# Optimization experiments

Measured on AMD Instinct MI355X. Metric: run time of the kernel, lower is better.

The kernel has to match this reference:

```python
import jax, jax.numpy as jnp
import numpy as np

N = 50000      # nodes
E = 800000     # edges (avg degree 16)
F_IN = 256
F_OUT = 256


def setup_inputs() -> dict:
    key = jax.random.key(0)
    ks = jax.random.split(key, 8)
    feature = jax.random.normal(ks[0], (N, F_IN), dtype=jnp.float32)
    e_w = jax.random.uniform(ks[1], (E, 1), dtype=jnp.float32)
    snorm_n = jnp.ones((N, 1), dtype=jnp.float32)
    snorm_e = jnp.ones((E, 1), dtype=jnp.float32)
    src = jax.random.randint(ks[2], (E,), 0, N, dtype=jnp.int32)
    dst = jax.random.randint(ks[3], (E,), 0, N, dtype=jnp.int32)
    scale = 1.0 / np.sqrt(F_IN)
    W_self = jax.random.normal(ks[4], (F_IN, F_OUT), dtype=jnp.float32) * scale
    W = jax.random.normal(ks[5], (F_IN, F_OUT), dtype=jnp.float32) * scale
    b = jax.random.normal(ks[6], (F_OUT,), dtype=jnp.float32) * scale
    return {"feature": feature, "e_w": e_w, "snorm_n": snorm_n,
            "snorm_e": snorm_e, "W_self": W_self, "W": W, "b": b,
            "src": src, "dst": dst}


def reference(feature, e_w, snorm_n, snorm_e, W_self, W, b, src, dst):
    n = feature.shape[0]
    ones_e = jnp.ones_like(src, dtype=feature.dtype)
    # self transform
    h_s = feature @ W_self                                   # [N, F_OUT]
    # source-side degree normalization: deg_out^{-1/2}
    out_deg = jnp.maximum(jax.ops.segment_sum(ones_e, src, num_segments=n), 1.0)
    feat = feature * (out_deg ** -0.5)[:, None]              # [N, F_IN]
    # message = h[src] * e_w, aggregated by sum into dst (u_mul_e + sum reduce)
    msgs = feat[src] * e_w                                   # [E, F_IN]
    agg = jax.ops.segment_sum(msgs, dst, num_segments=n)     # [N, F_IN]
    # neighbor transform + destination-side degree normalization
    h = agg @ W + b                                          # [N, F_OUT]
    in_deg = jnp.maximum(jax.ops.segment_sum(ones_e, dst, num_segments=n), 1.0)
    h = h * (in_deg ** -0.5)[:, None]
    return h_s + h, e_w
```

## Files before the change

kernel.cpp:

```cpp
#include <hip/hip_runtime.h>
#include <hip/hip_bf16.h>

#define N_NODES 50000
#define N_EDGES 800000

#define ROW_TILES    391
#define HIST_BLOCKS  782
#define GEMM_SPACE   1568
#define K1_BLOCKS    (HIST_BLOCKS + GEMM_SPACE)
#define WCONV_BLOCKS 512
#define SCAN_BLOCKS  196
#define EDGE_BLOCKS  782

typedef __bf16 bf16x8_t __attribute__((ext_vector_type(8)));
typedef float  f32x4_t  __attribute__((ext_vector_type(4)));
typedef unsigned short u16x8 __attribute__((ext_vector_type(8)));

__device__ __forceinline__ unsigned short f2bf(float x) {
  __hip_bfloat16 h = __float2bfloat16(x);
  return __builtin_bit_cast(unsigned short, h);
}
__device__ __forceinline__ float bf2f(unsigned short u) {
  unsigned int v = ((unsigned int)u) << 16;
  return __builtin_bit_cast(float, v);
}
__device__ __forceinline__ unsigned int pk2(float lo, float hi) {
  return ((unsigned int)f2bf(hi) << 16) | (unsigned int)f2bf(lo);
}

__global__ __launch_bounds__(256) void wconv_kernel(
    const float* __restrict__ Wself, const float* __restrict__ W,
    unsigned short* __restrict__ Bt)
{
  int idx = blockIdx.x * 256 + threadIdx.x;
  int n = idx >> 8, k = idx & 255;
  float v = (n < 256) ? Wself[k * 256 + n] : W[k * 256 + (n - 256)];
  Bt[idx] = f2bf(v);
}

__global__ __launch_bounds__(256, 4) void gemm_edge_kernel(
    const float* __restrict__ feature,
    const unsigned short* __restrict__ Bt,
    const float* __restrict__ e_w, const int* __restrict__ src, const int* __restrict__ dst,
    int* __restrict__ cnt_in, int* __restrict__ cnt_out,
    unsigned char* __restrict__ rank8, float* __restrict__ out1,
    unsigned short* __restrict__ hs16,
    unsigned char* __restrict__ y8)
{
  const int b   = blockIdx.x;
  const int tid = threadIdx.x;

  if (b < HIST_BLOCKS) {
    const int e0 = b * 1024 + tid;
#pragma unroll
    for (int k = 0; k < 4; ++k) {
      int e = e0 + k * 256;
      if (e < N_EDGES) {
        int s = src[e], d = dst[e];
        out1[e] = e_w[e];
        atomicAdd(&cnt_out[s], 1);
        rank8[e] = (unsigned char)atomicAdd(&cnt_in[d], 1);
      }
    }
    return;
  }

  const int u  = b - HIST_BLOCKS;
  const int q  = (u >> 3) & 3;
  const int t  = (u >> 5) * 8 + (((u & 7) + 6) & 7);
  if (t >= ROW_TILES) return;

  __shared__ __align__(16) unsigned short As[2][128 * 32];
  __shared__ __align__(16) unsigned short Bs[2][128 * 32];

  const int m0   = t * 128;
  const int bn0  = q * 128;
  const int lane = tid & 63;
  const int wave = tid >> 6;
  const int wm   = (wave & 1) * 64;
  const int wn   = (wave >> 1) * 64;
  const int fr   = lane & 15;
  const int fkc  = lane >> 4;

  const int ra = tid >> 1, ha = tid & 1;
  const int sA = (ra >> 1) & 3;
  const int arow = (m0 + ra < N_NODES) ? (m0 + ra) : 0;
  const float* aptr = feature + (size_t)arow * 256 + ha * 16;
  const int aw0 = ra * 32 + (((2 * ha) ^ sA) * 8);
  const int aw1 = ra * 32 + ((((2 * ha) | 1) ^ sA) * 8);

  f32x4_t acc[4][4] = {};

  {
#pragma unroll
    for (int i = 0; i < 2; ++i) {
      int r  = i * 64 + (tid >> 2);
      int cg = (tid & 3) ^ ((r >> 1) & 3);
      const unsigned short* gb = Bt + (size_t)(bn0 + r) * 256 + cg * 8;
      __builtin_amdgcn_global_load_lds((const __attribute__((address_space(1))) void*)gb,
                                       (__attribute__((address_space(3))) void*)&Bs[0][i * 2048 + wave * 512],
                                       16, 0, 0);
    }
    float4 a0 = *(const float4*)(aptr + 0);
    float4 a1 = *(const float4*)(aptr + 4);
    float4 a2 = *(const float4*)(aptr + 8);
    float4 a3 = *(const float4*)(aptr + 12);
    uint4 p0, p1;
    p0.x = pk2(a0.x, a0.y); p0.y = pk2(a0.z, a0.w);
    p0.z = pk2(a1.x, a1.y); p0.w = pk2(a1.z, a1.w);
    p1.x = pk2(a2.x, a2.y); p1.y = pk2(a2.z, a2.w);
    p1.z = pk2(a3.x, a3.y); p1.w = pk2(a3.z, a3.w);
    *(uint4*)&As[0][aw0] = p0;
    *(uint4*)&As[0][aw1] = p1;
  }
  __syncthreads();

#pragma unroll
  for (int s = 0; s < 8; ++s) {
    const int cb = s & 1, nb = cb ^ 1;
    float4 a0, a1, a2, a3;
    if (s < 7) {
      const int k0 = (s + 1) * 32;
#pragma unroll
      for (int i = 0; i < 2; ++i) {
        int r  = i * 64 + (tid >> 2);
        int cg = (tid & 3) ^ ((r >> 1) & 3);
        const unsigned short* gb = Bt + (size_t)(bn0 + r) * 256 + k0 + cg * 8;
        __builtin_amdgcn_global_load_lds((const __attribute__((address_space(1))) void*)gb,
                                         (__attribute__((address_space(3))) void*)&Bs[nb][i * 2048 + wave * 512],
                                         16, 0, 0);
      }
      a0 = *(const float4*)(aptr + k0 + 0);
      a1 = *(const float4*)(aptr + k0 + 4);
      a2 = *(const float4*)(aptr + k0 + 8);
      a3 = *(const float4*)(aptr + k0 + 12);
    }

    bf16x8_t af[4], bv[4];
#pragma unroll
    for (int i = 0; i < 4; ++i) {
      int R = wm + i * 16 + fr;
      af[i] = *(const bf16x8_t*)&As[cb][R * 32 + ((fkc ^ ((R >> 1) & 3)) * 8)];
    }
#pragma unroll
    for (int j = 0; j < 4; ++j) {
      int R = wn + j * 16 + fr;
      bv[j] = *(const bf16x8_t*)&Bs[cb][R * 32 + ((fkc ^ ((R >> 1) & 3)) * 8)];
    }
#pragma unroll
    for (int i = 0; i < 4; ++i)
#pragma unroll
      for (int j = 0; j < 4; ++j)
        acc[i][j] = __builtin_amdgcn_mfma_f32_16x16x32_bf16(af[i], bv[j], acc[i][j], 0, 0, 0);

    if (s < 7) {
      uint4 p0, p1;
      p0.x = pk2(a0.x, a0.y); p0.y = pk2(a0.z, a0.w);
      p0.z = pk2(a1.x, a1.y); p0.w = pk2(a1.z, a1.w);
      p1.x = pk2(a2.x, a2.y); p1.y = pk2(a2.z, a2.w);
      p1.z = pk2(a3.x, a3.y); p1.w = pk2(a3.z, a3.w);
      *(uint4*)&As[nb][aw0] = p0;
      *(uint4*)&As[nb][aw1] = p1;
      __syncthreads();
    }
  }

  if (q < 2) {
    const int cbase = q * 128 + wn + (lane & 15);
#pragma unroll
    for (int i = 0; i < 4; ++i) {
      int rowb = m0 + wm + i * 16 + (lane >> 4) * 4;
#pragma unroll
      for (int j = 0; j < 4; ++j) {
        int col = cbase + j * 16;
#pragma unroll
        for (int r = 0; r < 4; ++r) {
          int row = rowb + r;
          if (row < N_NODES)
            hs16[(size_t)row * 256 + col] = f2bf(acc[i][j][r]);
        }
      }
    }
  } else {
    const int cbase = (q - 2) * 128 + wn + (lane & 15);
#pragma unroll
    for (int i = 0; i < 4; ++i) {
      int rowb = m0 + wm + i * 16 + (lane >> 4) * 4;
#pragma unroll
      for (int j = 0; j < 4; ++j) {
        int col = cbase + j * 16;
#pragma unroll
        for (int r = 0; r < 4; ++r) {
          int row = rowb + r;
          if (row < N_NODES) {
            float ys = acc[i][j][r];
            unsigned int pk = (unsigned int)__builtin_amdgcn_cvt_pk_fp8_f32(ys, ys, 0, false);
            y8[(size_t)row * 256 + col] = (unsigned char)(pk & 0xffu);
          }
        }
      }
    }
  }
}

__global__ __launch_bounds__(256) void scan1_kernel(
    const int* __restrict__ cnt, int* __restrict__ sums)
{
  int idx = blockIdx.x * 256 + threadIdx.x;
  int v = (idx < N_NODES) ? cnt[idx] : 0;
#pragma unroll
  for (int d = 32; d; d >>= 1) v += __shfl_down(v, d);
  __shared__ int sm[4];
  if ((threadIdx.x & 63) == 0) sm[threadIdx.x >> 6] = v;
  __syncthreads();
  if (threadIdx.x == 0) sums[blockIdx.x] = sm[0] + sm[1] + sm[2] + sm[3];
}

__global__ __launch_bounds__(256) void scan2_kernel(int* __restrict__ sums)
{
  const int t = threadIdx.x;
  int v = (t < SCAN_BLOCKS) ? sums[t] : 0;
  __shared__ int sm[256];
  sm[t] = v;
  __syncthreads();
  for (int d = 1; d < 256; d <<= 1) {
    int u = (t >= d) ? sm[t - d] : 0;
    __syncthreads();
    sm[t] += u;
    __syncthreads();
  }
  if (t < SCAN_BLOCKS) sums[t] = sm[t] - v;
}

__global__ __launch_bounds__(256) void scan3_kernel(
    const int* __restrict__ cnt, const int* __restrict__ sums, int* __restrict__ off)
{
  const int t = threadIdx.x;
  int idx = blockIdx.x * 256 + t;
  int v = (idx < N_NODES) ? cnt[idx] : 0;
  __shared__ int sm[256];
  sm[t] = v;
  __syncthreads();
  for (int d = 1; d < 256; d <<= 1) {
    int u = (t >= d) ? sm[t - d] : 0;
    __syncthreads();
    sm[t] += u;
    __syncthreads();
  }
  if (idx <= N_NODES) off[idx] = sm[t] - v + sums[blockIdx.x];
}

__global__ __launch_bounds__(256) void scatter_kernel(
    const float* __restrict__ e_w, const int* __restrict__ src, const int* __restrict__ dst,
    const unsigned char* __restrict__ rank8, const int* __restrict__ off,
    unsigned int* __restrict__ csr)
{
  const int e0 = blockIdx.x * 1024 + threadIdx.x;
#pragma unroll
  for (int k = 0; k < 4; ++k) {
    int e = e0 + k * 256;
    if (e < N_EDGES) {
      int d = dst[e];
      int r = rank8[e];
      float w = e_w[e];
      int s = src[e];
      csr[off[d] + r] = ((unsigned int)f2bf(w) << 16) | (unsigned int)s;
    }
  }
}

__global__ __launch_bounds__(256) void agg_kernel(
    const unsigned char* __restrict__ y8, const unsigned int* __restrict__ csr,
    const int* __restrict__ off, const int* __restrict__ cnt_out,
    const unsigned short* __restrict__ hs16,
    const float* __restrict__ bias, float* __restrict__ out0)
{
  const int hw   = threadIdx.x >> 5;
  const int lane = threadIdx.x & 31;
  const int node = blockIdx.x * 8 + hw;
  if (node >= N_NODES) return;
  const int base = off[node];
  const int deg  = off[node + 1] - base;

  float a0 = 0.f, a1 = 0.f, a2 = 0.f, a3 = 0.f;
  float a4 = 0.f, a5 = 0.f, a6 = 0.f, a7 = 0.f;

  for (int bb = 0; bb < deg; bb += 32) {
    int idx = bb + lane;
    unsigned int ent = (idx < deg) ? csr[base + idx] : 0u;
    int   sl = (int)(ent & 0xffffu);
    float wl = bf2f((unsigned short)(ent >> 16));
    int co = cnt_out[sl]; if (co < 1) co = 1;
    wl *= rsqrtf((float)co);

#pragma unroll
    for (int t0 = 0; t0 < 32; t0 += 16) {
      if (bb + t0 >= deg) break;
#pragma unroll
      for (int t = 0; t < 16; ++t) {
        int eb = t0 + t;
        int   s = __shfl(sl, eb, 32);
        float w = __shfl(wl, eb, 32);
        uint2 u = *(const uint2*)(y8 + (size_t)s * 256 + lane * 8);
        a0 += w * __builtin_amdgcn_cvt_f32_fp8(u.x, 0);
        a1 += w * __builtin_amdgcn_cvt_f32_fp8(u.x, 1);
        a2 += w * __builtin_amdgcn_cvt_f32_fp8(u.x, 2);
        a3 += w * __builtin_amdgcn_cvt_f32_fp8(u.x, 3);
        a4 += w * __builtin_amdgcn_cvt_f32_fp8(u.y, 0);
        a5 += w * __builtin_amdgcn_cvt_f32_fp8(u.y, 1);
        a6 += w * __builtin_amdgcn_cvt_f32_fp8(u.y, 2);
        a7 += w * __builtin_amdgcn_cvt_f32_fp8(u.y, 3);
      }
    }
  }

  int dn = deg < 1 ? 1 : deg;
  float inv = rsqrtf((float)dn);
  size_t offo = (size_t)node * 256 + lane * 8;
  u16x8 hv = *(const u16x8*)(hs16 + offo);
  float4 b0 = *(const float4*)(bias + lane * 8);
  float4 b1 = *(const float4*)(bias + lane * 8 + 4);
  float4 o0, o1;
  o0.x = bf2f(hv[0]) + (a0 + b0.x) * inv;
  o0.y = bf2f(hv[1]) + (a1 + b0.y) * inv;
  o0.z = bf2f(hv[2]) + (a2 + b0.z) * inv;
  o0.w = bf2f(hv[3]) + (a3 + b0.w) * inv;
  o1.x = bf2f(hv[4]) + (a4 + b1.x) * inv;
  o1.y = bf2f(hv[5]) + (a5 + b1.y) * inv;
  o1.z = bf2f(hv[6]) + (a6 + b1.z) * inv;
  o1.w = bf2f(hv[7]) + (a7 + b1.w) * inv;
  *(float4*)(out0 + offo)     = o0;
  *(float4*)(out0 + offo + 4) = o1;
}

extern "C" void kernel_launch(void* const* d_in, const int* in_sizes, int n_in,
                              void* d_out, int out_size, void* d_ws, size_t ws_size,
                              hipStream_t stream) {
  const float* feature = (const float*)d_in[0];
  const float* e_w     = (const float*)d_in[1];
  const float* W_self  = (const float*)d_in[4];
  const float* W       = (const float*)d_in[5];
  const float* bias    = (const float*)d_in[6];
  const int*   src     = (const int*)d_in[7];
  const int*   dst     = (const int*)d_in[8];

  float* out0 = (float*)d_out;
  float* out1 = out0 + (size_t)N_NODES * 256;

  char* ws = (char*)d_ws;
  int*            cnt_in  = (int*)(ws + 0);
  int*            cnt_out = (int*)(ws + 262144);
  int*            off     = (int*)(ws + 524288);
  unsigned char*  rank8   = (unsigned char*)(ws + 786432);
  int*            sums    = (int*)(ws + 1638400);
  unsigned int*   csr     = (unsigned int*)(ws + 1835008);
  unsigned short* Bt      = (unsigned short*)(ws + 5242880);
  unsigned char*  y8      = (unsigned char*)(ws + 5767168);
  unsigned short* hs16    = (unsigned short*)(ws + 18567168);

  hipMemsetAsync(ws, 0, 524288, stream);

  wconv_kernel<<<WCONV_BLOCKS, 256, 0, stream>>>(W_self, W, Bt);
  gemm_edge_kernel<<<K1_BLOCKS, 256, 0, stream>>>(
      feature, Bt, e_w, src, dst, cnt_in, cnt_out, rank8, out1, hs16, y8);
  scan1_kernel<<<SCAN_BLOCKS, 256, 0, stream>>>(cnt_in, sums);
  scan2_kernel<<<1, 256, 0, stream>>>(sums);
  scan3_kernel<<<SCAN_BLOCKS, 256, 0, stream>>>(cnt_in, sums, off);
  scatter_kernel<<<EDGE_BLOCKS, 256, 0, stream>>>(e_w, src, dst, rank8, off, csr);
  agg_kernel<<<(N_NODES + 7) / 8, 256, 0, stream>>>(y8, csr, off, cnt_out, hs16, bias, out0);
}
```

Measured before the change: 283.5 us.

## Drop LDS staging in fused GEMM, load MFMA fragments directly from global

Removes the shared-memory double buffer and barriers from the GEMM part of the fused kernel. Each wave now loads its A (fp32, converted to bf16) and B fragments straight from global memory into registers. Histogram blocks are also interleaved with GEMM blocks in a 48-block pattern instead of all running first. This cuts LDS traffic and syncs and frees LDS for occupancy, at the cost of redundant global/L2 reads, since fragments are no longer shared across waves, and less latency hiding.

```diff
diff --git a/kernel.cpp b/kernel.cpp
--- a/kernel.cpp
+++ b/kernel.cpp
@@ -5,9 +5,7 @@
 #define N_EDGES 800000
 
 #define ROW_TILES    391
-#define HIST_BLOCKS  782
-#define GEMM_SPACE   1568
-#define K1_BLOCKS    (HIST_BLOCKS + GEMM_SPACE)
+#define K1_BLOCKS    2352
 #define WCONV_BLOCKS 512
 #define SCAN_BLOCKS  196
 #define EDGE_BLOCKS  782
@@ -15,6 +13,7 @@
 typedef __bf16 bf16x8_t __attribute__((ext_vector_type(8)));
 typedef float  f32x4_t  __attribute__((ext_vector_type(4)));
 typedef unsigned short u16x8 __attribute__((ext_vector_type(8)));
+typedef unsigned int   u32x4 __attribute__((ext_vector_type(4)));
 
 __device__ __forceinline__ unsigned short f2bf(float x) {
   __hip_bfloat16 h = __float2bfloat16(x);
@@ -26,6 +25,12 @@
 }
 __device__ __forceinline__ unsigned int pk2(float lo, float hi) {
   return ((unsigned int)f2bf(hi) << 16) | (unsigned int)f2bf(lo);
+}
+__device__ __forceinline__ bf16x8_t cvt8(float4 lo, float4 hi) {
+  u32x4 u;
+  u.x = pk2(lo.x, lo.y); u.y = pk2(lo.z, lo.w);
+  u.z = pk2(hi.x, hi.y); u.w = pk2(hi.z, hi.w);
+  return __builtin_bit_cast(bf16x8_t, u);
 }
 
 __global__ __launch_bounds__(256) void wconv_kernel(
@@ -49,9 +54,14 @@
 {
   const int b   = blockIdx.x;
   const int tid = threadIdx.x;
-
-  if (b < HIST_BLOCKS) {
-    const int e0 = b * 1024 + tid;
+  const int w   = b / 48;
+  const int o   = (b % 48) >> 3;
+  const int r   = b & 7;
+
+  if (o == 2 || o == 5) {
+    const int h = w * 16 + r + ((o == 5) ? 8 : 0);
+    if (h >= EDGE_BLOCKS) return;
+    const int e0 = h * 1024 + tid;
 #pragma unroll
     for (int k = 0; k < 4; ++k) {
       int e = e0 + k * 256;
@@ -65,13 +75,9 @@
     return;
   }
 
-  const int u  = b - HIST_BLOCKS;
-  const int q  = (u >> 3) & 3;
-  const int t  = (u >> 5) * 8 + (((u & 7) + 6) & 7);
+  const int q = o - (o > 2 ? 1 : 0);
+  const int t = w * 8 + r;
   if (t >= ROW_TILES) return;
-
-  __shared__ __align__(16) unsigned short As[2][128 * 32];
-  __shared__ __align__(16) unsigned short Bs[2][128 * 32];
 
   const int m0   = t * 128;
   const int bn0  = q * 128;
@@ -82,87 +88,37 @@
   const int fr   = lane & 15;
   const int fkc  = lane >> 4;
 
-  const int ra = tid >> 1, ha = tid & 1;
-  const int sA = (ra >> 1) & 3;
-  const int arow = (m0 + ra < N_NODES) ? (m0 + ra) : 0;
-  const float* aptr = feature + (size_t)arow * 256 + ha * 16;
-  const int aw0 = ra * 32 + (((2 * ha) ^ sA) * 8);
-  const int aw1 = ra * 32 + ((((2 * ha) | 1) ^ sA) * 8);
+  const float* ap[4];
+  const unsigned short* bp[4];
+#pragma unroll
+  for (int i = 0; i < 4; ++i) {
+    int row = m0 + wm + i * 16 + fr;
+    row = (row < N_NODES) ? row : 0;
+    ap[i] = feature + (size_t)row * 256 + fkc * 8;
+  }
+#pragma unroll
+  for (int j = 0; j < 4; ++j)
+    bp[j] = Bt + (size_t)(bn0 + wn + j * 16 + fr) * 256 + fkc * 8;
 
   f32x4_t acc[4][4] = {};
 
-  {
-#pragma unroll
-    for (int i = 0; i < 2; ++i) {
-      int r  = i * 64 + (tid >> 2);
-      int cg = (tid & 3) ^ ((r >> 1) & 3);
-      const unsigned short* gb = Bt + (size_t)(bn0 + r) * 256 + cg * 8;
-      __builtin_amdgcn_global_load_lds((const __attribute__((address_space(1))) void*)gb,
-                                       (__attribute__((address_space(3))) void*)&Bs[0][i * 2048 + wave * 512],
-                                       16, 0, 0);
-    }
-    float4 a0 = *(const float4*)(aptr + 0);
-    float4 a1 = *(const float4*)(aptr + 4);
-    float4 a2 = *(const float4*)(aptr + 8);
-    float4 a3 = *(const float4*)(aptr + 12);
-    uint4 p0, p1;
-    p0.x = pk2(a0.x, a0.y); p0.y = pk2(a0.z, a0.w);
-    p0.z = pk2(a1.x, a1.y); p0.w = pk2(a1.z, a1.w);
-    p1.x = pk2(a2.x, a2.y); p1.y = pk2(a2.z, a2.w);
-    p1.z = pk2(a3.x, a3.y); p1.w = pk2(a3.z, a3.w);
-    *(uint4*)&As[0][aw0] = p0;
-    *(uint4*)&As[0][aw1] = p1;
-  }
-  __syncthreads();
-
-#pragma unroll
   for (int s = 0; s < 8; ++s) {
-    const int cb = s & 1, nb = cb ^ 1;
-    float4 a0, a1, a2, a3;
-    if (s < 7) {
-      const int k0 = (s + 1) * 32;
-#pragma unroll
-      for (int i = 0; i < 2; ++i) {
-        int r  = i * 64 + (tid >> 2);
-        int cg = (tid & 3) ^ ((r >> 1) & 3);
-        const unsigned short* gb = Bt + (size_t)(bn0 + r) * 256 + k0 + cg * 8;
-        __builtin_amdgcn_global_load_lds((const __attribute__((address_space(1))) void*)gb,
-                                         (__attribute__((address_space(3))) void*)&Bs[nb][i * 2048 + wave * 512],
-                                         16, 0, 0);
-      }
-      a0 = *(const float4*)(aptr + k0 + 0);
-      a1 = *(const float4*)(aptr + k0 + 4);
-      a2 = *(const float4*)(aptr + k0 + 8);
-      a3 = *(const float4*)(aptr + k0 + 12);
-    }
-
-    bf16x8_t af[4], bv[4];
+    const int k0 = s * 32;
+    bf16x8_t av[4], bv[4];
 #pragma unroll
     for (int i = 0; i < 4; ++i) {
-      int R = wm + i * 16 + fr;
-      af[i] = *(const bf16x8_t*)&As[cb][R * 32 + ((fkc ^ ((R >> 1) & 3)) * 8)];
-    }
-#pragma unroll
-    for (int j = 0; j < 4; ++j) {
-      int R = wn + j * 16 + fr;
-      bv[j] = *(const bf16x8_t*)&Bs[cb][R * 32 + ((fkc ^ ((R >> 1) & 3)) * 8)];
-    }
+      float4 lo = *(const float4*)(ap[i] + k0);
+      float4 hi = *(const float4*)(ap[i] + k0 + 4);
+      av[i] = cvt8(lo, hi);
+    }
+#pragma unroll
+    for (int j = 0; j < 4; ++j)
+      bv[j] = *(const bf16x8_t*)(bp[j] + k0);
 #pragma unroll
     for (int i = 0; i < 4; ++i)
 #pragma unroll
       for (int j = 0; j < 4; ++j)
-        acc[i][j] = __builtin_amdgcn_mfma_f32_16x16x32_bf16(af[i], bv[j], acc[i][j], 0, 0, 0);
-
-    if (s < 7) {
-      uint4 p0, p1;
-      p0.x = pk2(a0.x, a0.y); p0.y = pk2(a0.z, a0.w);
-      p0.z = pk2(a1.x, a1.y); p0.w = pk2(a1.z, a1.w);
-      p1.x = pk2(a2.x, a2.y); p1.y = pk2(a2.z, a2.w);
-      p1.z = pk2(a3.x, a3.y); p1.w = pk2(a3.z, a3.w);
-      *(uint4*)&As[nb][aw0] = p0;
-      *(uint4*)&As[nb][aw1] = p1;
-      __syncthreads();
-    }
+        acc[i][j] = __builtin_amdgcn_mfma_f32_16x16x32_bf16(av[i], bv[j], acc[i][j], 0, 0, 0);
   }
 
   if (q < 2) {
@@ -174,10 +130,10 @@
       for (int j = 0; j < 4; ++j) {
         int col = cbase + j * 16;
 #pragma unroll
-        for (int r = 0; r < 4; ++r) {
-          int row = rowb + r;
+        for (int rr = 0; rr < 4; ++rr) {
+          int row = rowb + rr;
           if (row < N_NODES)
-            hs16[(size_t)row * 256 + col] = f2bf(acc[i][j][r]);
+            hs16[(size_t)row * 256 + col] = f2bf(acc[i][j][rr]);
         }
       }
     }
@@ -190,10 +146,10 @@
       for (int j = 0; j < 4; ++j) {
         int col = cbase + j * 16;
 #pragma unroll
-        for (int r = 0; r < 4; ++r) {
-          int row = rowb + r;
+        for (int rr = 0; rr < 4; ++rr) {
+          int row = rowb + rr;
           if (row < N_NODES) {
-            float ys = acc[i][j][r];
+            float ys = acc[i][j][rr];
             unsigned int pk = (unsigned int)__builtin_amdgcn_cvt_pk_fp8_f32(ys, ys, 0, false);
             y8[(size_t)row * 256 + col] = (unsigned char)(pk & 0xffu);
           }
```

Measured after the change: 304.8 us. 7.5% more time.
